# Optimization experiments

Hardware: AMD Instinct MI355X
Metric: run time of the kernel (lower is better)

The kernel has to match this reference:

```python
import jax, jax.numpy as jnp
import numpy as np
from jax import lax

N = 50000
C = 8
HW = 11
E = 800000
BD = 4
LIN_DIM = C * (HW - 2) * (HW - 2) + BD  # 652
HID = 256
OUT = 5
EPS = 1e-5


def _layernorm(h, g, b):
    mu = jnp.mean(h, axis=-1, keepdims=True)
    var = jnp.var(h, axis=-1, keepdims=True)
    return (h - mu) * lax.rsqrt(var + EPS) * g + b


def setup_inputs() -> dict:
    key = jax.random.key(0)
    ks = jax.random.split(key, 20)
    x = jax.random.normal(ks[0], (N, C, HW, HW), dtype=jnp.float32)
    bd_pred = jax.random.normal(ks[1], (N, BD), dtype=jnp.float32)
    src = jax.random.randint(ks[2], (E,), 0, N)
    dst = jax.random.randint(ks[3], (E,), 0, N)
    dst = jnp.where(src == dst, (dst + 1) % N, dst)  # no self loops
    edge_index = jnp.stack([src, dst]).astype(jnp.int64)
    s = 0.02
    p = {
        'conv_self_w': jax.random.normal(ks[4], (C, C, 3, 3), jnp.float32) * s,
        'conv_self_b': jnp.zeros((C,), jnp.float32),
        'lin_w': jax.random.normal(ks[5], (HID, LIN_DIM), jnp.float32) * s,
        'lin_b': jnp.zeros((HID,), jnp.float32),
        'lin_self_w': jax.random.normal(ks[6], (HID, LIN_DIM), jnp.float32) * s,
        'lin_self_b': jnp.zeros((HID,), jnp.float32),
        'sage_l_w': jax.random.normal(ks[7], (3, HID, HID), jnp.float32) * s,
        'sage_l_b': jnp.zeros((3, HID), jnp.float32),
        'sage_r_w': jax.random.normal(ks[8], (3, HID, HID), jnp.float32) * s,
        'ln_g': jnp.ones((2, HID), jnp.float32),
        'ln_b': jnp.zeros((2, HID), jnp.float32),
        'mp1_w': jax.random.normal(ks[9], (HID, HID), jnp.float32) * s,
        'mp1_b': jnp.zeros((HID,), jnp.float32),
        'mp2_w': jax.random.normal(ks[10], (OUT, HID), jnp.float32) * s,
        'mp2_b': jnp.zeros((OUT,), jnp.float32),
    }
    return dict(x=x, bd_pred=bd_pred, edge_index=edge_index, **p)


def reference(x, bd_pred, edge_index, conv_self_w, conv_self_b, lin_w, lin_b,
              lin_self_w, lin_self_b, sage_l_w, sage_l_b, sage_r_w,
              ln_g, ln_b, mp1_w, mp1_b, mp2_w, mp2_b):
    n = x.shape[0]
    src, dst = edge_index[0], edge_index[1]

    # CustomConv layer 0: conv_self -> flatten -> hstack(bd_pred) -> relu -> two linears
    h = lax.conv_general_dilated(x, conv_self_w, (1, 1), 'VALID',
                                 dimension_numbers=('NCHW', 'OIHW', 'NCHW'))
    h = h + conv_self_b[None, :, None, None]
    h = jnp.concatenate([h.reshape(n, -1), bd_pred], axis=1)  # [N, 652]
    h = jax.nn.relu(h)
    self_x = h @ lin_self_w.T + lin_self_b
    neigh = h @ lin_w.T + lin_b
    h = self_x + jax.ops.segment_sum(neigh[src], dst, num_segments=n)  # aggr='add'

    # in-degree for SAGEConv mean aggregation
    deg = jax.ops.segment_sum(jnp.ones((src.shape[0],), h.dtype), dst, num_segments=n)
    deg = jnp.maximum(deg, 1.0)[:, None]

    emb = h
    for i in range(3):  # SAGEConv layers 1..3
        mean_agg = jax.ops.segment_sum(h[src], dst, num_segments=n) / deg
        h = mean_agg @ sage_l_w[i].T + sage_l_b[i] + h @ sage_r_w[i].T
        emb = h
        h = jax.nn.relu(h)
        # dropout p=0.25 is identity in eval mode
        if i != 2:
            h = _layernorm(h, ln_g[i], ln_b[i])

    z = h @ mp1_w.T + mp1_b
    z = z @ mp2_w.T + mp2_b
    return emb, jax.nn.log_softmax(z, axis=1)
```

## Files before the change

kernel.cpp:

```cpp
#include <hip/hip_runtime.h>
#include <hip/hip_bf16.h>
#include <stdint.h>

#define NN 50000
#define EE 800000

typedef unsigned short u16;
typedef __attribute__((ext_vector_type(4))) float f32x4;
typedef __attribute__((ext_vector_type(8))) short bf16x8;

__device__ __forceinline__ float bu2f(u16 u){ return __uint_as_float(((unsigned)u)<<16); }
__device__ __forceinline__ u16 f2bu(float f){
  unsigned u = __float_as_uint(f);
  u += 0x7fffu + ((u>>16)&1u);
  return (u16)(u>>16);
}
__device__ __forceinline__ float lo16f(unsigned u){ return __uint_as_float(u << 16); }
__device__ __forceinline__ float hi16f(unsigned u){ return __uint_as_float(u & 0xffff0000u); }

__global__ void sniff_kernel(const int* __restrict__ e, const u16* __restrict__ xu,
                             int* __restrict__ flags){
  __shared__ int nz, cnt;
  int t = threadIdx.x;
  if (t == 0){ nz = 0; cnt = 0; }
  __syncthreads();
  if (e[2*t + 1] != 0) atomicOr(&nz, 1);
  u16 u = xu[2*t];
  int ef = (u >> 7) & 0xFF;
  int ok = (u == 0) || (ef >= 118 && ef <= 132);
  atomicAdd(&cnt, ok);
  __syncthreads();
  if (t == 0){ flags[0] = (nz == 0) ? 1 : 0; flags[1] = (cnt >= 200) ? 1 : 0; }
}

__global__ void convert_edges_kernel(const void* __restrict__ ep, int* __restrict__ outp,
                                     const int* __restrict__ flags, int total){
  int i = blockIdx.x*256 + threadIdx.x;
  if (i >= total) return;
  if (flags[0]) outp[i] = (int)((const long long*)ep)[i];
  else          outp[i] = ((const int*)ep)[i];
}

struct CanonTab {
  const void* src[15];
  void*       dst[15];
  int rows[15];
  int sk[15];
  int dk[15];
  int tobf[15];
};

__global__ __launch_bounds__(256) void canon_params_kernel(CanonTab tab, const int* __restrict__ flags){
  int a = blockIdx.y;
  int isbf = flags[1];
  int rows = tab.rows[a], sk = tab.sk[a], dk = tab.dk[a], tobf = tab.tobf[a];
  int n = rows * dk;
  int base = (blockIdx.x*256 + threadIdx.x) * 8;
  if (base >= n) return;
  #pragma unroll
  for (int uu = 0; uu < 8; uu++){
    int i = base + uu;
    if (i >= n) break;
    int r = i / dk, c = i - r*dk;
    float v = 0.f;
    if (c < sk){
      size_t si = (size_t)r*sk + c;
      v = isbf ? bu2f(((const u16*)tab.src[a])[si]) : ((const float*)tab.src[a])[si];
    }
    if (tobf) ((u16*)tab.dst[a])[i] = f2bu(v);
    else      ((float*)tab.dst[a])[i] = v;
  }
}

#define CROW_LOAD(R) { _Pragma("unroll") for (int q = 0; q < 11; q++) R[q] = xrow[xb + q]; xb += 11; }
#define CACC9(A,B,C,LOI) { _Pragma("unroll") for (int oj = 0; oj < 9; oj++){ \
    acc[(LOI)*9+oj] += A[oj]*w[0] + A[oj+1]*w[1] + A[oj+2]*w[2] \
                     + B[oj]*w[3] + B[oj+1]*w[4] + B[oj+2]*w[5] \
                     + C[oj]*w[6] + C[oj+1]*w[7] + C[oj+2]*w[8]; } }

__global__ __launch_bounds__(256, 2) void conv_relu_kernel(
    const void* __restrict__ xraw, const void* __restrict__ bdraw,
    const float* __restrict__ cw, const float* __restrict__ cb,
    const int* __restrict__ flags, u16* __restrict__ h0){
  __shared__ float xs[15488];
  __shared__ float wsm[576];
  __shared__ float bs[8];
  int t = threadIdx.x;
  int nb = blockIdx.x << 4;
  int isbf = flags[1];
  if (t < 144){ float4 u = ((const float4*)cw)[t]; wsm[4*t]=u.x; wsm[4*t+1]=u.y; wsm[4*t+2]=u.z; wsm[4*t+3]=u.w; }
  if (t < 8) bs[t] = cb[t];
  if (isbf){
    const u16* xg = (const u16*)xraw + (size_t)nb*968;
    for (int i = t; i < 1936; i += 256){
      uint4 v = *(const uint4*)(xg + (size_t)i*8);
      float* d = xs + i*8;
      d[0]=lo16f(v.x); d[1]=hi16f(v.x); d[2]=lo16f(v.y); d[3]=hi16f(v.y);
      d[4]=lo16f(v.z); d[5]=hi16f(v.z); d[6]=lo16f(v.w); d[7]=hi16f(v.w);
    }
  } else {
    const float* xg = (const float*)xraw + (size_t)nb*968;
    for (int i = t; i < 3872; i += 256)
      *(float4*)&xs[i*4] = *(const float4*)(xg + (size_t)i*4);
  }
  for (int i = t; i < 16*56; i += 256){
    int node = i / 56, c = i - node*56;
    u16 v = 0;
    if (c < 4){
      float f = isbf ? bu2f(((const u16*)bdraw)[(size_t)(nb+node)*4 + c])
                     : ((const float*)bdraw)[(size_t)(nb+node)*4 + c];
      v = f2bu(fmaxf(f, 0.f));
    }
    h0[(size_t)(nb+node)*704 + 648 + c] = v;
  }
  __syncthreads();
  int half = t >> 7;
  int idx  = t & 127;
  int node = idx >> 3, co = idx & 7;
  const float* xrow = xs + node*968;
  float binit = bs[co];
  if (half == 0){
    float acc[36];
    #pragma unroll
    for (int p = 0; p < 36; p++) acc[p] = binit;
    for (int ci = 0; ci < 8; ci++){
      float w[9];
      #pragma unroll
      for (int q = 0; q < 9; q++) w[q] = wsm[co*72 + ci*9 + q];
      int xb = ci*121;
      float r0[11], r1[11], r2[11];
      CROW_LOAD(r0) CROW_LOAD(r1) CROW_LOAD(r2) CACC9(r0,r1,r2,0)
      CROW_LOAD(r0) CACC9(r1,r2,r0,1)
      CROW_LOAD(r1) CACC9(r2,r0,r1,2)
      CROW_LOAD(r2) CACC9(r0,r1,r2,3)
    }
    u16* outr = h0 + (size_t)(nb+node)*704 + co*81;
    #pragma unroll
    for (int p = 0; p < 36; p++) outr[p] = f2bu(fmaxf(acc[p], 0.f));
  } else {
    float acc[45];
    #pragma unroll
    for (int p = 0; p < 45; p++) acc[p] = binit;
    for (int ci = 0; ci < 8; ci++){
      float w[9];
      #pragma unroll
      for (int q = 0; q < 9; q++) w[q] = wsm[co*72 + ci*9 + q];
      int xb = ci*121 + 44;
      float r0[11], r1[11], r2[11];
      CROW_LOAD(r0) CROW_LOAD(r1) CROW_LOAD(r2) CACC9(r0,r1,r2,0)
      CROW_LOAD(r0) CACC9(r1,r2,r0,1)
      CROW_LOAD(r1) CACC9(r2,r0,r1,2)
      CROW_LOAD(r2) CACC9(r0,r1,r2,3)
      CROW_LOAD(r0) CACC9(r1,r2,r0,4)
    }
    u16* outr = h0 + (size_t)(nb+node)*704 + co*81 + 36;
    #pragma unroll
    for (int p = 0; p < 45; p++) outr[p] = f2bu(fmaxf(acc[p], 0.f));
  }
}

__global__ void deg_kernel(const int* __restrict__ dst, int* __restrict__ degI, int E){
  int e = blockIdx.x*256 + threadIdx.x;
  if (e < E) atomicAdd(&degI[dst[e]], 1);
}
__global__ void invdeg_kernel(const int* __restrict__ degI, float* __restrict__ inv, int n){
  int i = blockIdx.x*256 + threadIdx.x;
  if (i < n){ int d = degI[i]; inv[i] = 1.0f / (float)(d > 1 ? d : 1); }
}

__global__ __launch_bounds__(1024) void scan_kernel(const int* __restrict__ degI,
                                                    int* __restrict__ rowptr,
                                                    int* __restrict__ cursor, int n){
  __shared__ int warp_sums[16];
  __shared__ int carry;
  int t = threadIdx.x;
  if (t == 0) carry = 0;
  __syncthreads();
  for (int base = 0; base < n; base += 8192){
    int i0 = base + t*8;
    int v[8]; int s = 0;
    #pragma unroll
    for (int q = 0; q < 8; q++){ int idx = i0+q; v[q] = (idx < n) ? degI[idx] : 0; s += v[q]; }
    int ts = s;
    #pragma unroll
    for (int off = 1; off < 64; off <<= 1){ int u = __shfl_up(ts, off); if ((t & 63) >= off) ts += u; }
    if ((t & 63) == 63) warp_sums[t >> 6] = ts;
    __syncthreads();
    if (t < 16){
      int wsv = warp_sums[t];
      #pragma unroll
      for (int off = 1; off < 16; off <<= 1){ int u = __shfl_up(wsv, off); if (t >= off) wsv += u; }
      warp_sums[t] = wsv;
    }
    __syncthreads();
    int blk = (t >= 64) ? warp_sums[(t >> 6) - 1] : 0;
    int excl = carry + blk + ts - s;
    #pragma unroll
    for (int q = 0; q < 8; q++){
      int idx = i0+q;
      if (idx < n){ rowptr[idx] = excl; cursor[idx] = excl; }
      excl += v[q];
    }
    int total = warp_sums[15];
    __syncthreads();
    if (t == 0) carry += total;
    __syncthreads();
  }
  if (t == 0) rowptr[n] = carry;
}

__global__ void bucket_kernel(const int* __restrict__ esrc, const int* __restrict__ edst,
                              int* __restrict__ cursor, int* __restrict__ ebuc, int E){
  int e = blockIdx.x*256 + threadIdx.x;
  if (e < E){ int pos = atomicAdd(&cursor[edst[e]], 1); ebuc[pos] = esrc[e]; }
}

#define GACC(U) { acc[0] += lo16f(U.x); acc[1] += hi16f(U.x); \
                  acc[2] += lo16f(U.y); acc[3] += hi16f(U.y); \
                  acc[4] += lo16f(U.z); acc[5] += hi16f(U.z); \
                  acc[6] += lo16f(U.w); acc[7] += hi16f(U.w); }
__global__ __launch_bounds__(256) void gather_agg_kernel(
    const u16* __restrict__ src_feat, int s_stride,
    const u16* __restrict__ addbase, int a_stride,
    const float* __restrict__ scale, u16* __restrict__ outp,
    const int* __restrict__ rowptr, const int* __restrict__ ebuc){
  int wid = threadIdx.x >> 6, lane = threadIdx.x & 63;
  int n = blockIdx.x*4 + wid;
  if (n >= NN) return;
  int half = lane >> 5;
  int sub  = lane & 31;
  int c0 = sub * 8;
  int beg = rowptr[n], end = rowptr[n+1];
  float acc[8] = {0.f,0.f,0.f,0.f,0.f,0.f,0.f,0.f};
  int j = beg + half;
  for (; j + 6 < end; j += 8){
    int s0 = ebuc[j], s1 = ebuc[j+2], s2 = ebuc[j+4], s3 = ebuc[j+6];
    uint4 u0 = *(const uint4*)(src_feat + (size_t)s0*s_stride + c0);
    uint4 u1 = *(const uint4*)(src_feat + (size_t)s1*s_stride + c0);
    uint4 u2 = *(const uint4*)(src_feat + (size_t)s2*s_stride + c0);
    uint4 u3 = *(const uint4*)(src_feat + (size_t)s3*s_stride + c0);
    GACC(u0) GACC(u1) GACC(u2) GACC(u3)
  }
  for (; j + 2 < end; j += 4){
    int s0 = ebuc[j], s1 = ebuc[j+2];
    uint4 u0 = *(const uint4*)(src_feat + (size_t)s0*s_stride + c0);
    uint4 u1 = *(const uint4*)(src_feat + (size_t)s1*s_stride + c0);
    GACC(u0) GACC(u1)
  }
  for (; j < end; j += 2){
    int s0 = ebuc[j];
    uint4 u0 = *(const uint4*)(src_feat + (size_t)s0*s_stride + c0);
    GACC(u0)
  }
  #pragma unroll
  for (int q = 0; q < 8; q++) acc[q] += __shfl_xor(acc[q], 32);
  if (half == 0){
    float sc = scale ? scale[n] : 1.f;
    #pragma unroll
    for (int q = 0; q < 8; q++) acc[q] *= sc;
    if (addbase){
      uint4 b = *(const uint4*)(addbase + (size_t)n*a_stride + c0);
      GACC(b)
    }
    uint4 o;
    o.x = (unsigned)f2bu(acc[0]) | ((unsigned)f2bu(acc[1]) << 16);
    o.y = (unsigned)f2bu(acc[2]) | ((unsigned)f2bu(acc[3]) << 16);
    o.z = (unsigned)f2bu(acc[4]) | ((unsigned)f2bu(acc[5]) << 16);
    o.w = (unsigned)f2bu(acc[6]) | ((unsigned)f2bu(acc[7]) << 16);
    *(uint4*)(outp + (size_t)n*256 + c0) = o;
  }
}

__global__ __launch_bounds__(256) void gemm_mfma_kernel(
    const u16* __restrict__ A1, int lda1, const u16* __restrict__ W1, int K1,
    const u16* __restrict__ A2, int lda2, const u16* __restrict__ W2, int K2,
    const float* __restrict__ bias, int ldc,
    u16* __restrict__ out_bf,
    void* __restrict__ out_emb,
    u16* __restrict__ out_relu_bf,
    const int* __restrict__ flags, int M){
  __shared__ u16 Asm[128][72];
  __shared__ u16 Wsm[128][72];
  int t = threadIdx.x;
  int wave = t >> 6, lane = t & 63;
  int wr = wave >> 1, wc = wave & 1;
  int m0 = blockIdx.x << 7;
  int o0 = blockIdx.y << 7;
  int lrow = t >> 1;
  int lk8  = (t & 1) << 3;
  int fr = lane & 15;
  int fkb = (lane >> 4) << 3;
  f32x4 acc[4][4] = {};

  for (int pass = 0; pass < 2; ++pass){
    const u16* A; const u16* W; int K, lda;
    if (pass == 0){ A = A1; W = W1; K = K1; lda = lda1; }
    else { if (!A2) break; A = A2; W = W2; K = K2; lda = lda2; }
    for (int k0 = 0; k0 < K; k0 += 64){
      int gm = m0 + lrow;
      int4 av0 = make_int4(0,0,0,0), av1 = av0, av2 = av0, av3 = av0;
      if (gm < M){
        const int4* ap = (const int4*)(A + (size_t)gm*lda + k0 + lk8);
        av0 = ap[0]; av1 = ap[2]; av2 = ap[4]; av3 = ap[6];
      }
      const int4* wp = (const int4*)(W + (size_t)(o0 + lrow)*K + k0 + lk8);
      int4 wv0 = wp[0], wv1 = wp[2], wv2 = wp[4], wv3 = wp[6];
      *(int4*)&Asm[lrow][lk8]      = av0;
      *(int4*)&Asm[lrow][lk8+16]   = av1;
      *(int4*)&Asm[lrow][lk8+32]   = av2;
      *(int4*)&Asm[lrow][lk8+48]   = av3;
      *(int4*)&Wsm[lrow][lk8]      = wv0;
      *(int4*)&Wsm[lrow][lk8+16]   = wv1;
      *(int4*)&Wsm[lrow][lk8+32]   = wv2;
      *(int4*)&Wsm[lrow][lk8+48]   = wv3;
      __syncthreads();
      #pragma unroll
      for (int kk = 0; kk < 2; kk++){
        int fk = kk*32 + fkb;
        bf16x8 af[4], wf[4];
        #pragma unroll
        for (int i = 0; i < 4; i++) af[i] = *(const bf16x8*)&Asm[wr*64 + i*16 + fr][fk];
        #pragma unroll
        for (int jj = 0; jj < 4; jj++) wf[jj] = *(const bf16x8*)&Wsm[wc*64 + jj*16 + fr][fk];
        #pragma unroll
        for (int i = 0; i < 4; i++)
          #pragma unroll
          for (int jj = 0; jj < 4; jj++)
            acc[i][jj] = __builtin_amdgcn_mfma_f32_16x16x32_bf16(af[i], wf[jj], acc[i][jj], 0, 0, 0);
      }
      __syncthreads();
    }
  }
  int isbf = flags[1];
  int fg = lane >> 4;
  #pragma unroll
  for (int i = 0; i < 4; i++){
    int rbase = m0 + wr*64 + i*16 + fg*4;
    #pragma unroll
    for (int jj = 0; jj < 4; jj++){
      int col = o0 + wc*64 + jj*16 + fr;
      float bv = bias[col];
      #pragma unroll
      for (int r = 0; r < 4; r++){
        int row = rbase + r;
        if (row < M){
          float v = acc[i][jj][r] + bv;
          size_t off = (size_t)row*ldc + col;
          if (out_bf)   out_bf[off] = f2bu(v);
          if (out_emb){
            if (isbf) ((u16*)out_emb)[off] = f2bu(v);
            else      ((float*)out_emb)[off] = v;
          }
          if (out_relu_bf) out_relu_bf[off] = f2bu(fmaxf(v, 0.f));
        }
      }
    }
  }
}

__global__ __launch_bounds__(256) void relu_ln_kernel(
    const u16* __restrict__ inb, u16* __restrict__ outb,
    const float* __restrict__ g, const float* __restrict__ b){
  __shared__ float rs[4], rs2[4];
  int n = blockIdx.x, t = threadIdx.x;
  float v = fmaxf(bu2f(inb[(size_t)n*256 + t]), 0.f);
  float s = v, s2 = v*v;
  #pragma unroll
  for (int off = 1; off < 64; off <<= 1){ s += __shfl_xor(s, off); s2 += __shfl_xor(s2, off); }
  if ((t & 63) == 0){ rs[t>>6] = s; rs2[t>>6] = s2; }
  __syncthreads();
  float S  = rs[0]+rs[1]+rs[2]+rs[3];
  float S2 = rs2[0]+rs2[1]+rs2[2]+rs2[3];
  float mu  = S * (1.f/256.f);
  float var = S2 * (1.f/256.f) - mu*mu;
  float inv = rsqrtf(var + 1e-5f);
  outb[(size_t)n*256 + t] = f2bu((v - mu) * inv * g[t] + b[t]);
}

__global__ __launch_bounds__(256) void head_kernel(
    const u16* __restrict__ z1, const float* __restrict__ w2, const float* __restrict__ b2,
    void* __restrict__ outbase, size_t out_off, const int* __restrict__ flags, int M){
  __shared__ float wsm[1280];
  __shared__ float bs[5];
  int t = threadIdx.x;
  for (int i = t; i < 320; i += 256){
    float4 u = ((const float4*)w2)[i];
    wsm[4*i]=u.x; wsm[4*i+1]=u.y; wsm[4*i+2]=u.z; wsm[4*i+3]=u.w;
  }
  if (t < 5) bs[t] = b2[t];
  __syncthreads();
  int n = blockIdx.x*256 + t;
  if (n >= M) return;
  const u16* zp = z1 + (size_t)n*256;
  float acc[5];
  #pragma unroll
  for (int o = 0; o < 5; o++) acc[o] = bs[o];
  for (int k = 0; k < 256; k += 4){
    ushort4 zu = *(const ushort4*)(zp + k);
    float z0 = bu2f(zu.x), z1f = bu2f(zu.y), z2 = bu2f(zu.z), z3 = bu2f(zu.w);
    #pragma unroll
    for (int o = 0; o < 5; o++){
      const float* w = wsm + o*256 + k;
      acc[o] += z0*w[0] + z1f*w[1] + z2*w[2] + z3*w[3];
    }
  }
  float mx = acc[0];
  #pragma unroll
  for (int o = 1; o < 5; o++) mx = fmaxf(mx, acc[o]);
  float se = 0.f;
  #pragma unroll
  for (int o = 0; o < 5; o++) se += expf(acc[o] - mx);
  float lse = mx + logf(se);
  int isbf = flags[1];
  if (isbf){
    u16* op = (u16*)outbase + out_off + (size_t)n*5;
    #pragma unroll
    for (int o = 0; o < 5; o++) op[o] = f2bu(acc[o] - lse);
  } else {
    float* op = (float*)outbase + out_off + (size_t)n*5;
    #pragma unroll
    for (int o = 0; o < 5; o++) op[o] = acc[o] - lse;
  }
}

extern "C" void kernel_launch(void* const* d_in, const int* in_sizes, int n_in,
                              void* d_out, int out_size, void* d_ws, size_t ws_size,
                              hipStream_t stream){
  (void)in_sizes; (void)n_in; (void)out_size; (void)ws_size;
  const void* x    = d_in[0];
  const void* bd   = d_in[1];
  const void* eraw = d_in[2];

  char* ws = (char*)d_ws;
  const size_t OFF_H0 = 0;
  const size_t OFF_A  = OFF_H0 + (size_t)NN*704*2;
  const size_t OFF_B  = OFF_A  + (size_t)NN*256*2;
  const size_t OFF_C  = OFF_B  + (size_t)NN*256*2;
  const size_t OFF_DEG= OFF_C  + (size_t)NN*256*2;
  const size_t OFF_INV= OFF_DEG + (size_t)NN*4;
  const size_t OFF_EDG= OFF_INV + (size_t)NN*4;
  const size_t OFF_RP = OFF_EDG + (size_t)2*EE*4;
  const size_t OFF_CUR= OFF_RP  + (size_t)(NN+16)*4;
  const size_t OFF_EBU= OFF_CUR + (size_t)NN*4;
  const size_t OFF_FLG= OFF_EBU + (size_t)EE*4;
  const size_t OFF_PRM= OFF_FLG + 256;

  u16*   h0   = (u16*)(ws + OFF_H0);
  u16*   bufA = (u16*)(ws + OFF_A);
  u16*   bufB = (u16*)(ws + OFF_B);
  u16*   bufC = (u16*)(ws + OFF_C);
  u16*   bufAB= (u16*)(ws + OFF_B);
  int*   degI = (int*)(ws + OFF_DEG);
  float* invd = (float*)(ws + OFF_INV);
  int*   edg  = (int*)(ws + OFF_EDG);
  int*   rowp = (int*)(ws + OFF_RP);
  int*   curs = (int*)(ws + OFF_CUR);
  int*   ebuc = (int*)(ws + OFF_EBU);
  int*   flg  = (int*)(ws + OFF_FLG);
  char*  prm  = ws + OFF_PRM;
  const int* esrc = edg;
  const int* edst = edg + EE;

  static const int crows[15] = {1,1,256,1,256,1,1,1,1,1,1,1,1,1,1};
  static const int csk[15]   = {576,8,652,256,652,256,196608,768,196608,512,512,65536,256,1280,5};
  static const int cdk[15]   = {576,8,704,256,704,256,196608,768,196608,512,512,65536,256,1280,5};
  static const int ctobf[15] = {0,0,1,0,1,0,1,0,1,0,0,1,0,0,0};
  CanonTab tab;
  size_t po = 0;
  void* dsts[15];
  for (int i = 0; i < 15; i++){
    tab.src[i] = d_in[3+i];
    tab.rows[i] = crows[i]; tab.sk[i] = csk[i]; tab.dk[i] = cdk[i]; tab.tobf[i] = ctobf[i];
    dsts[i] = prm + po;
    tab.dst[i] = dsts[i];
    size_t bytes = (size_t)crows[i]*cdk[i] * (ctobf[i] ? 2 : 4);
    po += (bytes + 63) & ~(size_t)63;
  }
  u16*   c_l2w = (u16*)(prm + po);  po += (size_t)512*704*2;
  float* c_l2b = (float*)(prm + po); po += 512*4 + 64;
  tab.dst[4] = c_l2w;
  tab.dst[2] = c_l2w + (size_t)256*704;
  tab.dst[5] = c_l2b;
  tab.dst[3] = c_l2b + 256;

  const float* c_cw  = (const float*)dsts[0];
  const float* c_cb  = (const float*)dsts[1];
  const u16*   c_slw = (const u16*)dsts[6];
  const float* c_slb = (const float*)dsts[7];
  const u16*   c_srw = (const u16*)dsts[8];
  const float* c_lng = (const float*)dsts[9];
  const float* c_lnb = (const float*)dsts[10];
  const u16*   c_m1w = (const u16*)dsts[11];
  const float* c_m1b = (const float*)dsts[12];
  const float* c_m2w = (const float*)dsts[13];
  const float* c_m2b = (const float*)dsts[14];

  hipMemsetAsync(degI, 0, (size_t)NN*4, stream);
  sniff_kernel<<<1, 256, 0, stream>>>((const int*)eraw, (const u16*)x, flg);
  {
    dim3 cgrid(96, 15);
    canon_params_kernel<<<cgrid, 256, 0, stream>>>(tab, flg);
  }
  convert_edges_kernel<<<(2*EE + 255)/256, 256, 0, stream>>>(eraw, edg, flg, 2*EE);
  conv_relu_kernel<<<NN/16, 256, 0, stream>>>(x, bd, c_cw, c_cb, flg, h0);
  deg_kernel<<<(EE + 255)/256, 256, 0, stream>>>(edst, degI, EE);
  invdeg_kernel<<<(NN + 255)/256, 256, 0, stream>>>(degI, invd, NN);
  scan_kernel<<<1, 1024, 0, stream>>>(degI, rowp, curs, NN);
  bucket_kernel<<<(EE + 255)/256, 256, 0, stream>>>(esrc, edst, curs, ebuc, EE);

  dim3 ggrid((NN + 127)/128, 2);
  dim3 ggrid0((NN + 127)/128, 4);
  const int agrid = (NN + 3)/4;
  gemm_mfma_kernel<<<ggrid0, 256, 0, stream>>>(h0, 704, c_l2w, 704,
      nullptr, 0, nullptr, 0, c_l2b, 512, bufAB, nullptr, nullptr, flg, NN);
  gather_agg_kernel<<<agrid, 256, 0, stream>>>(bufAB + 256, 512, bufAB, 512,
      nullptr, bufA, rowp, ebuc);

  for (int i = 0; i < 3; i++){
    gather_agg_kernel<<<agrid, 256, 0, stream>>>(bufA, 256, nullptr, 0,
        invd, bufC, rowp, ebuc);
    const u16*   L  = c_slw + (size_t)i*256*256;
    const float* Lb = c_slb + (size_t)i*256;
    const u16*   R  = c_srw + (size_t)i*256*256;
    if (i < 2){
      gemm_mfma_kernel<<<ggrid, 256, 0, stream>>>(bufC, 256, L, 256,
          bufA, 256, R, 256, Lb, 256, bufB, nullptr, nullptr, flg, NN);
      relu_ln_kernel<<<NN, 256, 0, stream>>>(bufB, bufA,
          c_lng + (size_t)i*256, c_lnb + (size_t)i*256);
    } else {
      gemm_mfma_kernel<<<ggrid, 256, 0, stream>>>(bufC, 256, L, 256,
          bufA, 256, R, 256, Lb, 256, nullptr, d_out, bufB, flg, NN);
    }
  }
  gemm_mfma_kernel<<<ggrid, 256, 0, stream>>>(bufB, 256, c_m1w, 256,
      nullptr, 0, nullptr, 0, c_m1b, 256, bufC, nullptr, nullptr, flg, NN);
  head_kernel<<<(NN + 255)/256, 256, 0, stream>>>(bufC, c_m2w, c_m2b,
      d_out, (size_t)NN*256, flg, NN);
}
```

Measured before the change: 877.8 us.

## Fuse degree counting into edge conversion, fold invdeg into scan, bf16 conv smem

Degree atomics move into the edge-conversion kernel and the inverse-degree computation moves into the scan kernel, which removes two kernel launches and one extra pass over the dst array. The conv kernel now stores its input tile in shared memory as bf16 with rows padded to 12 elements, and reads each row with 8-byte vector loads. This halves LDS footprint, which may allow more blocks per CU. For fp32 inputs it also rounds x to bf16 before the convolution, a precision loss relative to the reference, and the scatter into shared memory now needs per-element integer division.

```diff
diff --git a/kernel.cpp b/kernel.cpp
--- a/kernel.cpp
+++ b/kernel.cpp
@@ -34,11 +34,15 @@
 }
 
 __global__ void convert_edges_kernel(const void* __restrict__ ep, int* __restrict__ outp,
+                                     int* __restrict__ degI,
                                      const int* __restrict__ flags, int total){
   int i = blockIdx.x*256 + threadIdx.x;
   if (i >= total) return;
-  if (flags[0]) outp[i] = (int)((const long long*)ep)[i];
-  else          outp[i] = ((const int*)ep)[i];
+  int v;
+  if (flags[0]) v = (int)((const long long*)ep)[i];
+  else          v = ((const int*)ep)[i];
+  outp[i] = v;
+  if (i >= EE) atomicAdd(&degI[v], 1);
 }
 
 struct CanonTab {
@@ -72,7 +76,15 @@
   }
 }
 
-#define CROW_LOAD(R) { _Pragma("unroll") for (int q = 0; q < 11; q++) R[q] = xrow[xb + q]; xb += 11; }
+#define XND 1096
+#define CROW_LOAD(R) { \
+  uint2 p0 = *(const uint2*)&xrow[xb]; \
+  uint2 p1 = *(const uint2*)&xrow[xb+4]; \
+  uint2 p2 = *(const uint2*)&xrow[xb+8]; \
+  R[0]=lo16f(p0.x); R[1]=hi16f(p0.x); R[2]=lo16f(p0.y); R[3]=hi16f(p0.y); \
+  R[4]=lo16f(p1.x); R[5]=hi16f(p1.x); R[6]=lo16f(p1.y); R[7]=hi16f(p1.y); \
+  R[8]=lo16f(p2.x); R[9]=hi16f(p2.x); R[10]=lo16f(p2.y); \
+  xb += 12; }
 #define CACC9(A,B,C,LOI) { _Pragma("unroll") for (int oj = 0; oj < 9; oj++){ \
     acc[(LOI)*9+oj] += A[oj]*w[0] + A[oj+1]*w[1] + A[oj+2]*w[2] \
                      + B[oj]*w[3] + B[oj+1]*w[4] + B[oj+2]*w[5] \
@@ -82,7 +94,7 @@
     const void* __restrict__ xraw, const void* __restrict__ bdraw,
     const float* __restrict__ cw, const float* __restrict__ cb,
     const int* __restrict__ flags, u16* __restrict__ h0){
-  __shared__ float xs[15488];
+  __shared__ u16 xs[16*XND];
   __shared__ float wsm[576];
   __shared__ float bs[8];
   int t = threadIdx.x;
@@ -93,15 +105,35 @@
   if (isbf){
     const u16* xg = (const u16*)xraw + (size_t)nb*968;
     for (int i = t; i < 1936; i += 256){
-      uint4 v = *(const uint4*)(xg + (size_t)i*8);
-      float* d = xs + i*8;
-      d[0]=lo16f(v.x); d[1]=hi16f(v.x); d[2]=lo16f(v.y); d[3]=hi16f(v.y);
-      d[4]=lo16f(v.z); d[5]=hi16f(v.z); d[6]=lo16f(v.w); d[7]=hi16f(v.w);
+      ushort4 v0 = ((const ushort4*)xg)[2*i];
+      ushort4 v1 = ((const ushort4*)xg)[2*i+1];
+      u16 e[8] = {v0.x,v0.y,v0.z,v0.w,v1.x,v1.y,v1.z,v1.w};
+      int g = i*8;
+      #pragma unroll
+      for (int k = 0; k < 8; k++){
+        int gg = g + k;
+        int node = gg / 968, rem = gg - node*968;
+        int ci = rem / 121, rem2 = rem - ci*121;
+        int r = rem2 / 11, c = rem2 - r*11;
+        xs[node*XND + ci*132 + r*12 + c] = e[k];
+      }
     }
   } else {
     const float* xg = (const float*)xraw + (size_t)nb*968;
-    for (int i = t; i < 3872; i += 256)
-      *(float4*)&xs[i*4] = *(const float4*)(xg + (size_t)i*4);
+    for (int i = t; i < 1936; i += 256){
+      float4 u0 = ((const float4*)xg)[2*i];
+      float4 u1 = ((const float4*)xg)[2*i+1];
+      float e[8] = {u0.x,u0.y,u0.z,u0.w,u1.x,u1.y,u1.z,u1.w};
+      int g = i*8;
+      #pragma unroll
+      for (int k = 0; k < 8; k++){
+        int gg = g + k;
+        int node = gg / 968, rem = gg - node*968;
+        int ci = rem / 121, rem2 = rem - ci*121;
+        int r = rem2 / 11, c = rem2 - r*11;
+        xs[node*XND + ci*132 + r*12 + c] = f2bu(e[k]);
+      }
+    }
   }
   for (int i = t; i < 16*56; i += 256){
     int node = i / 56, c = i - node*56;
@@ -117,7 +149,7 @@
   int half = t >> 7;
   int idx  = t & 127;
   int node = idx >> 3, co = idx & 7;
-  const float* xrow = xs + node*968;
+  const u16* xrow = xs + node*XND;
   float binit = bs[co];
   if (half == 0){
     float acc[36];
@@ -127,7 +159,7 @@
       float w[9];
       #pragma unroll
       for (int q = 0; q < 9; q++) w[q] = wsm[co*72 + ci*9 + q];
-      int xb = ci*121;
+      int xb = ci*132;
       float r0[11], r1[11], r2[11];
       CROW_LOAD(r0) CROW_LOAD(r1) CROW_LOAD(r2) CACC9(r0,r1,r2,0)
       CROW_LOAD(r0) CACC9(r1,r2,r0,1)
@@ -145,7 +177,7 @@
       float w[9];
       #pragma unroll
       for (int q = 0; q < 9; q++) w[q] = wsm[co*72 + ci*9 + q];
-      int xb = ci*121 + 44;
+      int xb = ci*132 + 48;
       float r0[11], r1[11], r2[11];
       CROW_LOAD(r0) CROW_LOAD(r1) CROW_LOAD(r2) CACC9(r0,r1,r2,0)
       CROW_LOAD(r0) CACC9(r1,r2,r0,1)
@@ -159,18 +191,10 @@
   }
 }
 
-__global__ void deg_kernel(const int* __restrict__ dst, int* __restrict__ degI, int E){
-  int e = blockIdx.x*256 + threadIdx.x;
-  if (e < E) atomicAdd(&degI[dst[e]], 1);
-}
-__global__ void invdeg_kernel(const int* __restrict__ degI, float* __restrict__ inv, int n){
-  int i = blockIdx.x*256 + threadIdx.x;
-  if (i < n){ int d = degI[i]; inv[i] = 1.0f / (float)(d > 1 ? d : 1); }
-}
-
 __global__ __launch_bounds__(1024) void scan_kernel(const int* __restrict__ degI,
                                                     int* __restrict__ rowptr,
-                                                    int* __restrict__ cursor, int n){
+                                                    int* __restrict__ cursor,
+                                                    float* __restrict__ inv, int n){
   __shared__ int warp_sums[16];
   __shared__ int carry;
   int t = threadIdx.x;
@@ -198,7 +222,10 @@
     #pragma unroll
     for (int q = 0; q < 8; q++){
       int idx = i0+q;
-      if (idx < n){ rowptr[idx] = excl; cursor[idx] = excl; }
+      if (idx < n){
+        rowptr[idx] = excl; cursor[idx] = excl;
+        inv[idx] = 1.0f / (float)(v[q] > 1 ? v[q] : 1);
+      }
       excl += v[q];
     }
     int total = warp_sums[15];
@@ -501,11 +528,9 @@
     dim3 cgrid(96, 15);
     canon_params_kernel<<<cgrid, 256, 0, stream>>>(tab, flg);
   }
-  convert_edges_kernel<<<(2*EE + 255)/256, 256, 0, stream>>>(eraw, edg, flg, 2*EE);
+  convert_edges_kernel<<<(2*EE + 255)/256, 256, 0, stream>>>(eraw, edg, degI, flg, 2*EE);
   conv_relu_kernel<<<NN/16, 256, 0, stream>>>(x, bd, c_cw, c_cb, flg, h0);
-  deg_kernel<<<(EE + 255)/256, 256, 0, stream>>>(edst, degI, EE);
-  invdeg_kernel<<<(NN + 255)/256, 256, 0, stream>>>(degI, invd, NN);
-  scan_kernel<<<1, 1024, 0, stream>>>(degI, rowp, curs, NN);
+  scan_kernel<<<1, 1024, 0, stream>>>(degI, rowp, curs, invd, NN);
   bucket_kernel<<<(EE + 255)/256, 256, 0, stream>>>(esrc, edst, curs, ebuc, EE);
 
   dim3 ggrid((NN + 127)/128, 2);
```

New measurement: 887.9 us. About the same (+1.1%).
